# Performance work log

Hardware: AMD Instinct MI355X
Metric: run time of the kernel (lower is better)

## Reference

```python
import jax, jax.numpy as jnp
import numpy as np

M = 8          # ensemble size
B = 16384      # batch
HIST = 5       # history
L = 384        # latent_dim
A = 1          # action_dim
HID = 512      # hidden_dim
NHL = 2        # num_hidden_layers
DIN = L * HIST + A * HIST  # 1925
EPS = 1e-5     # BatchNorm eps


def setup_inputs() -> dict:
    key = jax.random.key(0)
    ks = jax.random.split(key, 6)
    w = lambda k, shape: (jax.random.normal(k, shape, jnp.float32) * 0.02)
    return {
        "z_hist": jax.random.normal(ks[0], (B, HIST, L), jnp.float32),
        "a_hist": jax.random.normal(ks[1], (B, HIST, A), jnp.float32),
        # per-model parameters, stacked along leading ensemble dim M
        "W1": w(ks[2], (M, DIN, HID)),
        "b1": jnp.zeros((M, HID), jnp.float32),
        "Wh": w(ks[3], (NHL, M, HID, HID)),
        "bh": jnp.zeros((NHL, M, HID), jnp.float32),
        "gamma": jnp.ones((NHL, M, HID), jnp.float32),
        "beta": jnp.zeros((NHL, M, HID), jnp.float32),
        "rmean": jnp.zeros((NHL, M, HID), jnp.float32),   # BN running mean (eval mode)
        "rvar": jnp.ones((NHL, M, HID), jnp.float32),      # BN running var (eval mode)
        "W3": w(ks[4], (M, HID, L)),
        "b3": jnp.zeros((M, L), jnp.float32),
    }


def reference(z_hist, a_hist, W1, b1, Wh, bh, gamma, beta, rmean, rvar, W3, b3):
    # EnsembleTransitionModel.forward, batched over the ensemble dim instead of
    # a Python loop over models. BatchNorm in eval mode; Dropout inactive (eval).
    bsz = z_hist.shape[0]
    x = jnp.concatenate([z_hist.reshape(bsz, -1), a_hist.reshape(bsz, -1)], axis=1)  # [B, DIN]
    # input projection + ReLU: [M, B, HID]
    h = jax.nn.relu(jnp.einsum('bi,mih->mbh', x, W1) + b1[:, None, :])
    n_layers = Wh.shape[0]
    for l in range(n_layers):  # small fixed structural loop (num_hidden_layers)
        h = jnp.einsum('mbh,mhk->mbk', h, Wh[l]) + bh[l][:, None, :]
        h = (h - rmean[l][:, None, :]) * jax.lax.rsqrt(rvar[l][:, None, :] + EPS)
        h = jax.nn.relu(h * gamma[l][:, None, :] + beta[l][:, None, :])
    delta = jnp.einsum('mbh,mhl->mbl', h, W3) + b3[:, None, :]
    # residual: pred_z = z_t + delta, broadcast over ensemble dim
    return delta + z_hist[:, -1, :][None, :, :]
```

## Files before the change

kernel.cpp:

```cpp
#include <hip/hip_runtime.h>
#include <hip/hip_bf16.h>

#define M_ENS 8
#define BATCH 16384
#define HIST 5
#define LDIM 384
#define HID 512
#define NHL 2
#define DIN 1925
#define KP 2048

typedef unsigned short u16;
typedef unsigned int u32;
typedef __attribute__((ext_vector_type(8))) short bf16x8;
typedef __attribute__((ext_vector_type(4))) float f32x4;

__device__ __forceinline__ u16 f2b(float f) {
    u32 u = __builtin_bit_cast(u32, f);
    u32 r = (u + 0x7fffu + ((u >> 16) & 1u)) >> 16;
    return (u16)r;
}

#define BARRIER asm volatile("s_barrier" ::: "memory")

__global__ void build_x(const float* __restrict__ z, const float* __restrict__ a,
                        u16* __restrict__ xp) {
    int idx = blockIdx.x * 256 + threadIdx.x;
    int b = idx / (KP / 2);
    int k2 = (idx % (KP / 2)) * 2;
    if (b >= BATCH) return;
    u32 packed = 0;
#pragma unroll
    for (int j = 0; j < 2; ++j) {
        int k = k2 + j;
        float v = 0.f;
        if (k < HIST * LDIM) v = z[(size_t)b * (HIST * LDIM) + k];
        else if (k < DIN)    v = a[b * HIST + (k - HIST * LDIM)];
        packed |= ((u32)f2b(v)) << (16 * j);
    }
    *(u32*)(&xp[(size_t)b * KP + k2]) = packed;
}

__global__ void transpose_cvt(const float* __restrict__ in, u16* __restrict__ out,
                              int R, int C, int Rp) {
    __shared__ float tile[32][33];
    const float* inb = in + (size_t)blockIdx.z * R * C;
    u16* outb = out + (size_t)blockIdx.z * C * Rp;
    int r0 = blockIdx.x * 32, c0 = blockIdx.y * 32;
    int tx = threadIdx.x & 31, ty = threadIdx.x >> 5;
#pragma unroll
    for (int i = 0; i < 32; i += 8) {
        int r = r0 + ty + i;
        float v = 0.f;
        if (r < R) v = inb[(size_t)r * C + c0 + tx];
        tile[ty + i][tx] = v;
    }
    __syncthreads();
#pragma unroll
    for (int i = 0; i < 32; i += 8) {
        outb[(size_t)(c0 + ty + i) * Rp + r0 + tx] = f2b(tile[tx][ty + i]);
    }
}

__global__ void make_tables(const float* __restrict__ bh, const float* __restrict__ gamma,
                            const float* __restrict__ beta, const float* __restrict__ rmean,
                            const float* __restrict__ rvar, float* __restrict__ s,
                            float* __restrict__ t, int n) {
    int i = blockIdx.x * 256 + threadIdx.x;
    if (i >= n) return;
    float inv = rsqrtf(rvar[i] + 1e-5f);
    float sc = gamma[i] * inv;
    s[i] = sc;
    t[i] = (bh[i] - rmean[i]) * sc + beta[i];
}

template <int MODE>
__global__ __launch_bounds__(512, 2) void gemm8p(
    const u16* __restrict__ A, const u16* __restrict__ Bw,
    const float* __restrict__ Sv, const float* __restrict__ Tv,
    u16* __restrict__ Ho, int K) {
    extern __shared__ char smem[];
    const int tid = threadIdx.x;
    const int lane = tid & 63;
    const int wid = tid >> 6;
    const int wm = wid >> 2;
    const int wn = wid & 3;

    int rowT, colT, mI;
    const u16 *Ab, *Bb;
    int lda, ldb;
    if (MODE == 0) {
        int xcd = blockIdx.x & 7, i = blockIdx.x >> 3;
        rowT = i >> 1; colT = xcd * 2 + (i & 1);
        Ab = A; lda = KP;
        Bb = Bw + (size_t)colT * 256 * KP; ldb = KP;
        mI = 0;
    } else {
        const int nwg = gridDim.x;
        const int swz = (blockIdx.x & 7) * (nwg >> 3) + (blockIdx.x >> 3);
        mI = swz >> 7;
        int rem = swz & 127;
        rowT = rem >> 1; colT = rem & 1;
        Ab = A + (size_t)mI * BATCH * HID; lda = HID;
        Bb = Bw + (size_t)mI * HID * HID + (size_t)colT * 256 * HID; ldb = HID;
    }
    const int rowBase = rowT * 256;
    const int NT = K >> 6;

    auto STAGE = [&](int par, int op, int half, int tk) {
#pragma unroll
        for (int i = 0; i < 2; ++i) {
            int ii = wid * 2 + i;
            int row = ii * 8 + (lane >> 3);
            int gc = lane & 7;
            const u16* src;
            if (op == 0)
                src = Ab + (size_t)(rowBase + half * 128 + row) * lda + tk * 64 + ((gc ^ (row & 7)) << 3);
            else
                src = Bb + (size_t)(half * 128 + row) * ldb + tk * 64 + ((gc ^ (row & 7)) << 3);
            u16* dst = (u16*)(smem + par * 65536 + op * 32768 + half * 16384) + (size_t)(ii * 64 + lane) * 8;
            __builtin_amdgcn_global_load_lds((const __attribute__((address_space(1))) void*)src,
                                             (__attribute__((address_space(3))) void*)dst, 16, 0, 0);
        }
    };

    const int laneRow = lane & 15;
    int xg[2];
    xg[0] = (((lane >> 4)) ^ (lane & 7)) << 4;
    xg[1] = ((4 | (lane >> 4)) ^ (lane & 7)) << 4;
#define RDF(base, r, kk) (*(const bf16x8*)((base) + (size_t)(r) * 128 + xg[kk]))

    f32x4 acc[8][4] = {};
    bf16x8 af[4][2], bfr[4][2];
    const int bcol0 = (wn & 1) * 64;

    STAGE(0, 1, 0, 0); STAGE(0, 1, 1, 0);
    STAGE(0, 0, 0, 0); STAGE(0, 0, 1, 0);
    if (NT > 1) { STAGE(1, 1, 0, 1); STAGE(1, 1, 1, 1); }
    asm volatile("s_waitcnt vmcnt(4)" ::: "memory");
    BARRIER;

    for (int T = 0; T < NT; ++T) {
        const int p = T & 1;
        const char* pA = smem + p * 65536 + wm * 16384;
        const char* pB = smem + p * 65536 + 32768 + (wn >> 1) * 16384;

#pragma unroll
        for (int mf = 0; mf < 4; ++mf) {
            af[mf][0] = RDF(pA, mf * 16 + laneRow, 0);
            af[mf][1] = RDF(pA, mf * 16 + laneRow, 1);
        }
#pragma unroll
        for (int nf = 0; nf < 2; ++nf) {
            bfr[nf][0] = RDF(pB, bcol0 + nf * 16 + laneRow, 0);
            bfr[nf][1] = RDF(pB, bcol0 + nf * 16 + laneRow, 1);
        }
        if (T + 1 < NT) STAGE((T + 1) & 1, 0, 0, T + 1);
        BARRIER;
        __builtin_amdgcn_s_setprio(1);
#pragma unroll
        for (int kk = 0; kk < 2; ++kk)
#pragma unroll
            for (int mf = 0; mf < 4; ++mf)
#pragma unroll
                for (int nf = 0; nf < 2; ++nf)
                    acc[mf][nf] = __builtin_amdgcn_mfma_f32_16x16x32_bf16(af[mf][kk], bfr[nf][kk], acc[mf][nf], 0, 0, 0);
        __builtin_amdgcn_s_setprio(0);
        BARRIER;

#pragma unroll
        for (int nf = 2; nf < 4; ++nf) {
            bfr[nf][0] = RDF(pB, bcol0 + nf * 16 + laneRow, 0);
            bfr[nf][1] = RDF(pB, bcol0 + nf * 16 + laneRow, 1);
        }
        if (T + 1 < NT) STAGE((T + 1) & 1, 0, 1, T + 1);
        BARRIER;
        __builtin_amdgcn_s_setprio(1);
#pragma unroll
        for (int kk = 0; kk < 2; ++kk)
#pragma unroll
            for (int mf = 0; mf < 4; ++mf)
#pragma unroll
                for (int nf = 2; nf < 4; ++nf)
                    acc[mf][nf] = __builtin_amdgcn_mfma_f32_16x16x32_bf16(af[mf][kk], bfr[nf][kk], acc[mf][nf], 0, 0, 0);
        __builtin_amdgcn_s_setprio(0);
        BARRIER;

#pragma unroll
        for (int mf = 0; mf < 4; ++mf) {
            af[mf][0] = RDF(pA, (4 + mf) * 16 + laneRow, 0);
            af[mf][1] = RDF(pA, (4 + mf) * 16 + laneRow, 1);
        }
        if (T + 2 < NT) STAGE(p, 1, 0, T + 2);
        BARRIER;
        __builtin_amdgcn_s_setprio(1);
#pragma unroll
        for (int kk = 0; kk < 2; ++kk)
#pragma unroll
            for (int mf = 0; mf < 4; ++mf)
#pragma unroll
                for (int nf = 2; nf < 4; ++nf)
                    acc[4 + mf][nf] = __builtin_amdgcn_mfma_f32_16x16x32_bf16(af[mf][kk], bfr[nf][kk], acc[4 + mf][nf], 0, 0, 0);
        __builtin_amdgcn_s_setprio(0);
        BARRIER;

        if (T + 2 < NT) {
            STAGE(p, 1, 1, T + 2);
            asm volatile("s_waitcnt vmcnt(4)" ::: "memory");
        } else {
            asm volatile("s_waitcnt vmcnt(0)" ::: "memory");
        }
        BARRIER;
        __builtin_amdgcn_s_setprio(1);
#pragma unroll
        for (int kk = 0; kk < 2; ++kk)
#pragma unroll
            for (int mf = 0; mf < 4; ++mf)
#pragma unroll
                for (int nf = 0; nf < 2; ++nf)
                    acc[4 + mf][nf] = __builtin_amdgcn_mfma_f32_16x16x32_bf16(af[mf][kk], bfr[nf][kk], acc[4 + mf][nf], 0, 0, 0);
        __builtin_amdgcn_s_setprio(0);
        BARRIER;
    }

#pragma unroll
    for (int mf = 0; mf < 8; ++mf) {
        int row = rowBase + wm * 128 + mf * 16 + ((lane >> 4) << 2);
#pragma unroll
        for (int nf = 0; nf < 4; ++nf) {
            int c = colT * 256 + wn * 64 + nf * 16 + (lane & 15);
            if (MODE == 0) {
                float tb = Tv[c];
                size_t base = (size_t)(c >> 9) * BATCH * HID + (c & 511);
#pragma unroll
                for (int q = 0; q < 4; ++q) {
                    float v = acc[mf][nf][q] + tb;
                    Ho[base + (size_t)(row + q) * HID] = f2b(v > 0.f ? v : 0.f);
                }
            } else {
                float sc = Sv[mI * HID + c], tb = Tv[mI * HID + c];
                u16* H = Ho + (size_t)mI * BATCH * HID;
#pragma unroll
                for (int q = 0; q < 4; ++q) {
                    float v = acc[mf][nf][q] * sc + tb;
                    H[(size_t)(row + q) * HID + c] = f2b(v > 0.f ? v : 0.f);
                }
            }
        }
    }
}

__global__ __launch_bounds__(512, 1) void h2out(
    const u16* __restrict__ h1, const u16* __restrict__ Wh2,
    const float* __restrict__ Sv, const float* __restrict__ Tv,
    const u16* __restrict__ W3p, const float* __restrict__ b3,
    const float* __restrict__ zres, float* __restrict__ out) {
    extern __shared__ char smem[];
    const int tid = threadIdx.x;
    const int lane = tid & 63;
    const int wid = tid >> 6;
    const int wm = wid >> 2;
    const int wn = wid & 3;
    const int m = blockIdx.x & 7;
    const int rowBase = (blockIdx.x >> 3) * 128;
    const int lr15 = lane & 15;

    const u16* Ab = h1 + ((size_t)m * BATCH + rowBase) * HID;
    const u16* Bb = Wh2 + (size_t)m * HID * HID;
    const u16* W3b = W3p + (size_t)m * LDIM * HID;
    const float* b3b = b3 + m * LDIM;

    int xg[2];
    xg[0] = (((lane >> 4)) ^ (lane & 7)) << 4;
    xg[1] = ((4 | (lane >> 4)) ^ (lane & 7)) << 4;

    auto stA = [&](int par, int tk) {
#pragma unroll
        for (int i = 0; i < 2; ++i) {
            int ii = wid * 2 + i;
            int row = ii * 8 + (lane >> 3);
            int gc = lane & 7;
            const u16* src = Ab + (size_t)row * HID + tk * 64 + ((gc ^ (row & 7)) << 3);
            u16* dst = (u16*)(smem + par * 16384) + (size_t)(ii * 64 + lane) * 8;
            __builtin_amdgcn_global_load_lds((const __attribute__((address_space(1))) void*)src,
                                             (__attribute__((address_space(3))) void*)dst, 16, 0, 0);
        }
    };
    auto stB = [&](int par, int q, int tk) {
#pragma unroll
        for (int i = 0; i < 2; ++i) {
            int ii = wid * 2 + i;
            int row = ii * 8 + (lane >> 3);
            int gc = lane & 7;
            const u16* src = Bb + (size_t)(q * 128 + row) * HID + tk * 64 + ((gc ^ (row & 7)) << 3);
            u16* dst = (u16*)(smem + 32768 + par * 65536 + q * 16384) + (size_t)(ii * 64 + lane) * 8;
            __builtin_amdgcn_global_load_lds((const __attribute__((address_space(1))) void*)src,
                                             (__attribute__((address_space(3))) void*)dst, 16, 0, 0);
        }
    };

    f32x4 acc[4][8] = {};
    bf16x8 afr[4][2];
    const int NT = HID / 64;

    stA(0, 0); stB(0, 0, 0); stB(0, 1, 0); stB(0, 2, 0); stB(0, 3, 0);
    asm volatile("s_waitcnt vmcnt(0)" ::: "memory");
    BARRIER;

    for (int T = 0; T < NT; ++T) {
        const int p = T & 1;
        const char* pA = smem + p * 16384;
        const char* qb = smem + 32768 + p * 65536 + wn * 16384;

#pragma unroll
        for (int mf = 0; mf < 4; ++mf) {
            int lr = wm * 64 + mf * 16 + lr15;
            afr[mf][0] = RDF(pA, lr, 0);
            afr[mf][1] = RDF(pA, lr, 1);
        }
        bf16x8 b01[2][2];
#pragma unroll
        for (int nf = 0; nf < 2; ++nf) {
            b01[nf][0] = RDF(qb, nf * 16 + lr15, 0);
            b01[nf][1] = RDF(qb, nf * 16 + lr15, 1);
        }
        if (T + 1 < NT) stA(p ^ 1, T + 1);
        BARRIER;
        __builtin_amdgcn_s_setprio(1);
#pragma unroll
        for (int kk = 0; kk < 2; ++kk)
#pragma unroll
            for (int mf = 0; mf < 4; ++mf)
#pragma unroll
                for (int nf = 0; nf < 2; ++nf)
                    acc[mf][nf] = __builtin_amdgcn_mfma_f32_16x16x32_bf16(afr[mf][kk], b01[nf][kk], acc[mf][nf], 0, 0, 0);
        __builtin_amdgcn_s_setprio(0);
        BARRIER;

#pragma unroll
        for (int nf = 0; nf < 2; ++nf) {
            b01[nf][0] = RDF(qb, (2 + nf) * 16 + lr15, 0);
            b01[nf][1] = RDF(qb, (2 + nf) * 16 + lr15, 1);
        }
        if (T + 1 < NT) { stB(p ^ 1, 0, T + 1); stB(p ^ 1, 1, T + 1); }
        BARRIER;
        __builtin_amdgcn_s_setprio(1);
#pragma unroll
        for (int kk = 0; kk < 2; ++kk)
#pragma unroll
            for (int mf = 0; mf < 4; ++mf)
#pragma unroll
                for (int nf = 0; nf < 2; ++nf)
                    acc[mf][2 + nf] = __builtin_amdgcn_mfma_f32_16x16x32_bf16(afr[mf][kk], b01[nf][kk], acc[mf][2 + nf], 0, 0, 0);
        __builtin_amdgcn_s_setprio(0);
        BARRIER;

#pragma unroll
        for (int nf = 0; nf < 2; ++nf) {
            b01[nf][0] = RDF(qb, (4 + nf) * 16 + lr15, 0);
            b01[nf][1] = RDF(qb, (4 + nf) * 16 + lr15, 1);
        }
        if (T + 1 < NT) { stB(p ^ 1, 2, T + 1); stB(p ^ 1, 3, T + 1); }
        BARRIER;
        __builtin_amdgcn_s_setprio(1);
#pragma unroll
        for (int kk = 0; kk < 2; ++kk)
#pragma unroll
            for (int mf = 0; mf < 4; ++mf)
#pragma unroll
                for (int nf = 0; nf < 2; ++nf)
                    acc[mf][4 + nf] = __builtin_amdgcn_mfma_f32_16x16x32_bf16(afr[mf][kk], b01[nf][kk], acc[mf][4 + nf], 0, 0, 0);
        __builtin_amdgcn_s_setprio(0);
        BARRIER;

#pragma unroll
        for (int nf = 0; nf < 2; ++nf) {
            b01[nf][0] = RDF(qb, (6 + nf) * 16 + lr15, 0);
            b01[nf][1] = RDF(qb, (6 + nf) * 16 + lr15, 1);
        }
        if (T + 2 < NT) {
            stA(p, T + 2);
            asm volatile("s_waitcnt vmcnt(2)" ::: "memory");
        } else {
            asm volatile("s_waitcnt vmcnt(0)" ::: "memory");
        }
        BARRIER;
        __builtin_amdgcn_s_setprio(1);
#pragma unroll
        for (int kk = 0; kk < 2; ++kk)
#pragma unroll
            for (int mf = 0; mf < 4; ++mf)
#pragma unroll
                for (int nf = 0; nf < 2; ++nf)
                    acc[mf][6 + nf] = __builtin_amdgcn_mfma_f32_16x16x32_bf16(afr[mf][kk], b01[nf][kk], acc[mf][6 + nf], 0, 0, 0);
        __builtin_amdgcn_s_setprio(0);
        BARRIER;
    }

#pragma unroll
    for (int mf = 0; mf < 4; ++mf) {
#pragma unroll
        for (int nf = 0; nf < 8; ++nf) {
            int col = wn * 128 + nf * 16 + lr15;
            float sc = Sv[m * HID + col], tt = Tv[m * HID + col];
#pragma unroll
            for (int q = 0; q < 4; ++q) {
                int row = wm * 64 + mf * 16 + ((lane >> 4) << 2) + q;
                float v = acc[mf][nf][q] * sc + tt;
                v = v > 0.f ? v : 0.f;
                *(u16*)(smem + 32768 + row * 1024 + (((col >> 3) ^ (row & 7)) << 4) + ((col & 7) << 1)) = f2b(v);
            }
        }
    }
    asm volatile("s_waitcnt lgkmcnt(0)" ::: "memory");
    BARRIER;

    bf16x8 w3r[3];
#pragma unroll
    for (int j = 0; j < 3; ++j) {
        int gi = tid * 3 + j;
        w3r[j] = *(const bf16x8*)(W3b + (size_t)(gi >> 2) * HID + ((gi & 3) << 3));
    }
    f32x4 acc2[4][6] = {};
    for (int t = 0; t < 16; ++t) {
#pragma unroll
        for (int j = 0; j < 3; ++j) {
            int gi = tid * 3 + j;
            *(bf16x8*)(smem + (gi >> 2) * 64 + (((gi & 3) ^ ((gi >> 2) & 3)) << 4)) = w3r[j];
        }
        if (t + 1 < 16) {
#pragma unroll
            for (int j = 0; j < 3; ++j) {
                int gi = tid * 3 + j;
                w3r[j] = *(const bf16x8*)(W3b + (size_t)(gi >> 2) * HID + (t + 1) * 32 + ((gi & 3) << 3));
            }
        }
        asm volatile("s_waitcnt lgkmcnt(0)" ::: "memory");
        BARRIER;
        bf16x8 a1[4], b1r[6];
#pragma unroll
        for (int mf = 0; mf < 4; ++mf) {
            int r = wm * 64 + mf * 16 + lr15;
            a1[mf] = *(const bf16x8*)(smem + 32768 + r * 1024 + (((4 * t + (lane >> 4)) ^ (lane & 7)) << 4));
        }
#pragma unroll
        for (int nf = 0; nf < 6; ++nf) {
            int r3 = wn * 96 + nf * 16 + lr15;
            b1r[nf] = *(const bf16x8*)(smem + r3 * 64 + (((lane >> 4) ^ (r3 & 3)) << 4));
        }
        __builtin_amdgcn_s_setprio(1);
#pragma unroll
        for (int mf = 0; mf < 4; ++mf)
#pragma unroll
            for (int nf = 0; nf < 6; ++nf)
                acc2[mf][nf] = __builtin_amdgcn_mfma_f32_16x16x32_bf16(a1[mf], b1r[nf], acc2[mf][nf], 0, 0, 0);
        __builtin_amdgcn_s_setprio(0);
        BARRIER;
    }

#pragma unroll
    for (int mf = 0; mf < 4; ++mf) {
#pragma unroll
        for (int nf = 0; nf < 6; ++nf) {
            int c = wn * 96 + nf * 16 + lr15;
            float bv = b3b[c];
#pragma unroll
            for (int q = 0; q < 4; ++q) {
                int grow = rowBase + wm * 64 + mf * 16 + ((lane >> 4) << 2) + q;
                out[((size_t)m * BATCH + grow) * LDIM + c] =
                    acc2[mf][nf][q] + bv + zres[(size_t)grow * (HIST * LDIM) + (HIST - 1) * LDIM + c];
            }
        }
    }
}

template <int MODE>
__global__ __launch_bounds__(256, 2) void gemm_bt(
    const u16* __restrict__ A, size_t aStride, int lda,
    const u16* __restrict__ Bt, size_t bStride,
    const float* __restrict__ Sv, const float* __restrict__ Tv, int ptStride,
    u16* __restrict__ Ho, size_t hStride,
    float* __restrict__ Fo, size_t fStride,
    const float* __restrict__ Zres,
    int K, int m0) {
    __shared__ u16 As[128 * 64];
    __shared__ u16 Bs[128 * 64];

    const int tid = threadIdx.x;
    const int lane = tid & 63;
    const int wid = tid >> 6;
    const int wr = (wid >> 1) * 64;
    const int wc = (wid & 1) * 64;
    const int z = blockIdx.z;
    const int rowBase = blockIdx.x * 128;
    const int colBase = blockIdx.y * 128;

    const u16* Ab = A + (size_t)z * aStride;
    const u16* Bb = Bt + (size_t)z * bStride;

    f32x4 acc[4][4] = {};

    int aoff[4], boff[4];
#pragma unroll
    for (int f = 0; f < 4; ++f) {
        int ar = wr + f * 16 + (lane & 15);
        aoff[f] = (ar * 128 + ((lane >> 4) * 16)) ^ ((ar & 7) << 4);
        int br = wc + f * 16 + (lane & 15);
        boff[f] = (br * 128 + ((lane >> 4) * 16)) ^ ((br & 7) << 4);
    }

    for (int k0 = 0; k0 < K; k0 += 64) {
#pragma unroll
        for (int i = 0; i < 4; ++i) {
            int gg = i * 256 + tid;
            int row = gg >> 3, gc = gg & 7;
            const u16* srcA = Ab + (size_t)(rowBase + row) * lda + k0 + ((gc ^ (row & 7)) << 3);
            __builtin_amdgcn_global_load_lds(
                (const __attribute__((address_space(1))) void*)srcA,
                (__attribute__((address_space(3))) void*)(As + gg * 8), 16, 0, 0);
            const u16* srcB = Bb + (size_t)(colBase + row) * K + k0 + ((gc ^ (row & 7)) << 3);
            __builtin_amdgcn_global_load_lds(
                (const __attribute__((address_space(1))) void*)srcB,
                (__attribute__((address_space(3))) void*)(Bs + gg * 8), 16, 0, 0);
        }
        __syncthreads();
#pragma unroll
        for (int kk = 0; kk < 2; ++kk) {
            bf16x8 af[4], bfr[4];
#pragma unroll
            for (int f = 0; f < 4; ++f) {
                af[f]  = *(const bf16x8*)((const char*)As + (aoff[f] ^ (kk << 6)));
                bfr[f] = *(const bf16x8*)((const char*)Bs + (boff[f] ^ (kk << 6)));
            }
#pragma unroll
            for (int i = 0; i < 4; ++i)
#pragma unroll
                for (int j = 0; j < 4; ++j)
                    acc[i][j] = __builtin_amdgcn_mfma_f32_16x16x32_bf16(af[i], bfr[j], acc[i][j], 0, 0, 0);
        }
        __syncthreads();
    }

    const int mg = m0 + z;
#pragma unroll
    for (int i = 0; i < 4; ++i) {
        int rbase = rowBase + wr + i * 16 + ((lane >> 4) << 2);
#pragma unroll
        for (int j = 0; j < 4; ++j) {
            int n = colBase + wc + j * 16 + (lane & 15);
            if (MODE == 0) {
                float bias = Tv[(size_t)mg * ptStride + n];
                u16* H = Ho + (size_t)z * hStride;
#pragma unroll
                for (int q = 0; q < 4; ++q) {
                    float v = acc[i][j][q] + bias;
                    v = v > 0.f ? v : 0.f;
                    H[(size_t)(rbase + q) * HID + n] = f2b(v);
                }
            } else if (MODE == 1) {
                float sc = Sv[(size_t)mg * ptStride + n];
                float tt = Tv[(size_t)mg * ptStride + n];
                u16* H = Ho + (size_t)z * hStride;
#pragma unroll
                for (int q = 0; q < 4; ++q) {
                    float v = acc[i][j][q] * sc + tt;
                    v = v > 0.f ? v : 0.f;
                    H[(size_t)(rbase + q) * HID + n] = f2b(v);
                }
            } else {
                float bias = Tv[(size_t)mg * ptStride + n];
                float* F = Fo + (size_t)z * fStride;
#pragma unroll
                for (int q = 0; q < 4; ++q) {
                    int b = rbase + q;
                    float v = acc[i][j][q] + bias + Zres[(size_t)b * (HIST * LDIM) + (HIST - 1) * LDIM + n];
                    F[(size_t)b * LDIM + n] = v;
                }
            }
        }
    }
}

extern "C" void kernel_launch(void* const* d_in, const int* in_sizes, int n_in,
                              void* d_out, int out_size, void* d_ws, size_t ws_size,
                              hipStream_t stream) {
    const float* z_hist = (const float*)d_in[0];
    const float* a_hist = (const float*)d_in[1];
    const float* W1    = (const float*)d_in[2];
    const float* b1    = (const float*)d_in[3];
    const float* Wh    = (const float*)d_in[4];
    const float* bh    = (const float*)d_in[5];
    const float* gamma = (const float*)d_in[6];
    const float* beta  = (const float*)d_in[7];
    const float* rmean = (const float*)d_in[8];
    const float* rvar  = (const float*)d_in[9];
    const float* W3    = (const float*)d_in[10];
    const float* b3    = (const float*)d_in[11];
    float* out = (float*)d_out;

    char* ws = (char*)d_ws;
    size_t off = 0;
    auto alloc = [&](size_t bytes) {
        void* p = ws + off;
        off = (off + bytes + 255) & ~(size_t)255;
        return p;
    };
    u16* xp  = (u16*)alloc((size_t)BATCH * KP * 2);
    u16* W1t = (u16*)alloc((size_t)M_ENS * HID * KP * 2);
    u16* Wht = (u16*)alloc((size_t)NHL * M_ENS * HID * HID * 2);
    u16* W3t = (u16*)alloc((size_t)M_ENS * LDIM * HID * 2);
    float* stab = (float*)alloc((size_t)NHL * M_ENS * HID * 4);
    float* ttab = (float*)alloc((size_t)NHL * M_ENS * HID * 4);
    size_t fixed = off;
    size_t hFull = (size_t)M_ENS * BATCH * HID * 2;
    bool full = (fixed + 2 * hFull <= ws_size);
    int MC = full ? M_ENS : 1;
    u16* h0 = (u16*)alloc((size_t)MC * BATCH * HID * 2);
    u16* h1 = (u16*)alloc((size_t)MC * BATCH * HID * 2);

    {
        int total = BATCH * KP / 2;
        build_x<<<(total + 255) / 256, 256, 0, stream>>>(z_hist, a_hist, xp);
        dim3 g1(KP / 32, HID / 32, M_ENS);
        transpose_cvt<<<g1, 256, 0, stream>>>(W1, W1t, DIN, HID, KP);
        dim3 g2(HID / 32, HID / 32, NHL * M_ENS);
        transpose_cvt<<<g2, 256, 0, stream>>>(Wh, Wht, HID, HID, HID);
        dim3 g3(HID / 32, LDIM / 32, M_ENS);
        transpose_cvt<<<g3, 256, 0, stream>>>(W3, W3t, HID, LDIM, HID);
        int n = NHL * M_ENS * HID;
        make_tables<<<(n + 255) / 256, 256, 0, stream>>>(bh, gamma, beta, rmean, rvar, stab, ttab, n);
    }

    if (full) {
        (void)hipFuncSetAttribute(reinterpret_cast<const void*>(&gemm8p<0>),
                                  hipFuncAttributeMaxDynamicSharedMemorySize, 131072);
        (void)hipFuncSetAttribute(reinterpret_cast<const void*>(&gemm8p<1>),
                                  hipFuncAttributeMaxDynamicSharedMemorySize, 131072);
        (void)hipFuncSetAttribute(reinterpret_cast<const void*>(&h2out),
                                  hipFuncAttributeMaxDynamicSharedMemorySize, 163840);
        gemm8p<0><<<1024, 512, 131072, stream>>>(xp, W1t, nullptr, b1, h0, KP);
        gemm8p<1><<<1024, 512, 131072, stream>>>(h0, Wht, stab, ttab, h1, HID);
        h2out<<<1024, 512, 163840, stream>>>(
            h1, Wht + (size_t)M_ENS * HID * HID,
            stab + M_ENS * HID, ttab + M_ENS * HID,
            W3t, b3, z_hist, out);
    } else {
        for (int m0 = 0; m0 < M_ENS; m0 += MC) {
            dim3 grid(BATCH / 128, HID / 128, MC);
            gemm_bt<0><<<grid, 256, 0, stream>>>(
                xp, 0, KP,
                W1t + (size_t)m0 * HID * KP, (size_t)HID * KP,
                nullptr, b1, HID,
                h0, (size_t)BATCH * HID, nullptr, 0, nullptr,
                KP, m0);
            for (int l = 0; l < NHL; ++l) {
                u16* hin = l ? h1 : h0;
                u16* hout = l ? h0 : h1;
                gemm_bt<1><<<grid, 256, 0, stream>>>(
                    hin, (size_t)BATCH * HID, HID,
                    Wht + ((size_t)l * M_ENS + m0) * HID * HID, (size_t)HID * HID,
                    stab + (size_t)l * M_ENS * HID, ttab + (size_t)l * M_ENS * HID, HID,
                    hout, (size_t)BATCH * HID, nullptr, 0, nullptr,
                    HID, m0);
            }
            dim3 gridO(BATCH / 128, LDIM / 128, MC);
            gemm_bt<2><<<gridO, 256, 0, stream>>>(
                h0, (size_t)BATCH * HID, HID,
                W3t + (size_t)m0 * LDIM * HID, (size_t)LDIM * HID,
                nullptr, b3, LDIM,
                nullptr, 0,
                out + (size_t)m0 * BATCH * LDIM, (size_t)BATCH * LDIM,
                z_hist,
                HID, m0);
        }
    }
}
```

Before: 626.5 us.

## Replace layer-1 pipelined 256x256 GEMM with simple 128x128 tile kernel

The first-layer GEMM (x[B,2048] times W1 for all 8 models, N=4096) moves from the double-buffered 256x256-tile gemm8p<0> with 512 threads to a new l1_bt kernel. The new kernel uses 128x128 tiles, 256 threads, static shared memory, 2 blocks per CU and an XCD-aware tile mapping. This trades the software pipelining and larger reuse per tile for smaller tiles, more blocks and better occupancy. The change also drops MODE 0 from gemm8p, adds a GLL macro, and changes one m0 argument in the fallback path from m0 to 0.

```diff
diff --git a/kernel.cpp b/kernel.cpp
--- a/kernel.cpp
+++ b/kernel.cpp
@@ -22,6 +22,9 @@
 }
 
 #define BARRIER asm volatile("s_barrier" ::: "memory")
+#define GLL(src, dst) __builtin_amdgcn_global_load_lds( \
+    (const __attribute__((address_space(1))) void*)(src), \
+    (__attribute__((address_space(3))) void*)(dst), 16, 0, 0)
 
 __global__ void build_x(const float* __restrict__ z, const float* __restrict__ a,
                         u16* __restrict__ xp) {
@@ -72,6 +75,84 @@
     float sc = gamma[i] * inv;
     s[i] = sc;
     t[i] = (bh[i] - rmean[i]) * sc + beta[i];
+}
+
+__global__ __launch_bounds__(256, 2) void l1_bt(
+    const u16* __restrict__ xp, const u16* __restrict__ W1t,
+    const float* __restrict__ b1, u16* __restrict__ Ho) {
+    __shared__ u16 As[128 * 64];
+    __shared__ u16 Bs[128 * 64];
+
+    const int tid = threadIdx.x;
+    const int lane = tid & 63;
+    const int wid = tid >> 6;
+    const int wr = (wid >> 1) * 64;
+    const int wc = (wid & 1) * 64;
+
+    const int bid = blockIdx.x;
+    const int xcd = bid & 7, i = bid >> 3;
+    const int colT = xcd * 4 + (i & 3);
+    const int rowT = i >> 2;
+    const int rowBase = rowT * 128;
+    const int colBase = colT * 128;
+
+    const u16* Ab = xp + (size_t)rowBase * KP;
+    const u16* Bb = W1t + (size_t)colBase * KP;
+
+    f32x4 acc[4][4] = {};
+
+    int aoff[4], boff[4];
+#pragma unroll
+    for (int f = 0; f < 4; ++f) {
+        int ar = wr + f * 16 + (lane & 15);
+        aoff[f] = (ar * 128 + ((lane >> 4) * 16)) ^ ((ar & 7) << 4);
+        int br = wc + f * 16 + (lane & 15);
+        boff[f] = (br * 128 + ((lane >> 4) * 16)) ^ ((br & 7) << 4);
+    }
+
+    for (int k0 = 0; k0 < KP; k0 += 64) {
+#pragma unroll
+        for (int s = 0; s < 4; ++s) {
+            int gg = s * 256 + tid;
+            int row = gg >> 3, gc = gg & 7;
+            const u16* srcA = Ab + (size_t)row * KP + k0 + ((gc ^ (row & 7)) << 3);
+            GLL(srcA, As + gg * 8);
+            const u16* srcB = Bb + (size_t)row * KP + k0 + ((gc ^ (row & 7)) << 3);
+            GLL(srcB, Bs + gg * 8);
+        }
+        __syncthreads();
+#pragma unroll
+        for (int kk = 0; kk < 2; ++kk) {
+            bf16x8 af[4], bfr[4];
+#pragma unroll
+            for (int f = 0; f < 4; ++f) {
+                af[f]  = *(const bf16x8*)((const char*)As + (aoff[f] ^ (kk << 6)));
+                bfr[f] = *(const bf16x8*)((const char*)Bs + (boff[f] ^ (kk << 6)));
+            }
+#pragma unroll
+            for (int a = 0; a < 4; ++a)
+#pragma unroll
+                for (int b = 0; b < 4; ++b)
+                    acc[a][b] = __builtin_amdgcn_mfma_f32_16x16x32_bf16(af[a], bfr[b], acc[a][b], 0, 0, 0);
+        }
+        __syncthreads();
+    }
+
+#pragma unroll
+    for (int a = 0; a < 4; ++a) {
+        int rbase = rowBase + wr + a * 16 + ((lane >> 4) << 2);
+#pragma unroll
+        for (int b = 0; b < 4; ++b) {
+            int c = colBase + wc + b * 16 + (lane & 15);
+            float tb = b1[c];
+            size_t base = (size_t)(c >> 9) * BATCH * HID + (c & 511);
+#pragma unroll
+            for (int q = 0; q < 4; ++q) {
+                float v = acc[a][b][q] + tb;
+                Ho[base + (size_t)(rbase + q) * HID] = f2b(v > 0.f ? v : 0.f);
+            }
+        }
+    }
 }
 
 template <int MODE>
@@ -86,24 +167,14 @@
     const int wm = wid >> 2;
     const int wn = wid & 3;
 
-    int rowT, colT, mI;
-    const u16 *Ab, *Bb;
-    int lda, ldb;
-    if (MODE == 0) {
-        int xcd = blockIdx.x & 7, i = blockIdx.x >> 3;
-        rowT = i >> 1; colT = xcd * 2 + (i & 1);
-        Ab = A; lda = KP;
-        Bb = Bw + (size_t)colT * 256 * KP; ldb = KP;
-        mI = 0;
-    } else {
-        const int nwg = gridDim.x;
-        const int swz = (blockIdx.x & 7) * (nwg >> 3) + (blockIdx.x >> 3);
-        mI = swz >> 7;
-        int rem = swz & 127;
-        rowT = rem >> 1; colT = rem & 1;
-        Ab = A + (size_t)mI * BATCH * HID; lda = HID;
-        Bb = Bw + (size_t)mI * HID * HID + (size_t)colT * 256 * HID; ldb = HID;
-    }
+    const int nwg = gridDim.x;
+    const int swz = (blockIdx.x & 7) * (nwg >> 3) + (blockIdx.x >> 3);
+    const int mI = swz >> 7;
+    const int rem = swz & 127;
+    const int rowT = rem >> 1, colT = rem & 1;
+    const u16* Ab = A + (size_t)mI * BATCH * HID;
+    const u16* Bb = Bw + (size_t)mI * HID * HID + (size_t)colT * 256 * HID;
+    const int lda = HID, ldb = HID;
     const int rowBase = rowT * 256;
     const int NT = K >> 6;
 
@@ -119,8 +190,7 @@
             else
                 src = Bb + (size_t)(half * 128 + row) * ldb + tk * 64 + ((gc ^ (row & 7)) << 3);
             u16* dst = (u16*)(smem + par * 65536 + op * 32768 + half * 16384) + (size_t)(ii * 64 + lane) * 8;
-            __builtin_amdgcn_global_load_lds((const __attribute__((address_space(1))) void*)src,
-                                             (__attribute__((address_space(3))) void*)dst, 16, 0, 0);
+            GLL(src, dst);
         }
     };
 
@@ -229,22 +299,12 @@
 #pragma unroll
         for (int nf = 0; nf < 4; ++nf) {
             int c = colT * 256 + wn * 64 + nf * 16 + (lane & 15);
-            if (MODE == 0) {
-                float tb = Tv[c];
-                size_t base = (size_t)(c >> 9) * BATCH * HID + (c & 511);
-#pragma unroll
-                for (int q = 0; q < 4; ++q) {
-                    float v = acc[mf][nf][q] + tb;
-                    Ho[base + (size_t)(row + q) * HID] = f2b(v > 0.f ? v : 0.f);
-                }
-            } else {
-                float sc = Sv[mI * HID + c], tb = Tv[mI * HID + c];
-                u16* H = Ho + (size_t)mI * BATCH * HID;
-#pragma unroll
-                for (int q = 0; q < 4; ++q) {
-                    float v = acc[mf][nf][q] * sc + tb;
-                    H[(size_t)(row + q) * HID + c] = f2b(v > 0.f ? v : 0.f);
-                }
+            float sc = Sv[mI * HID + c], tb = Tv[mI * HID + c];
+            u16* H = Ho + (size_t)mI * BATCH * HID;
+#pragma unroll
+            for (int q = 0; q < 4; ++q) {
+                float v = acc[mf][nf][q] * sc + tb;
+                H[(size_t)(row + q) * HID + c] = f2b(v > 0.f ? v : 0.f);
             }
         }
     }
@@ -282,8 +342,7 @@
             int gc = lane & 7;
             const u16* src = Ab + (size_t)row * HID + tk * 64 + ((gc ^ (row & 7)) << 3);
             u16* dst = (u16*)(smem + par * 16384) + (size_t)(ii * 64 + lane) * 8;
-            __builtin_amdgcn_global_load_lds((const __attribute__((address_space(1))) void*)src,
-                                             (__attribute__((address_space(3))) void*)dst, 16, 0, 0);
+            GLL(src, dst);
         }
     };
     auto stB = [&](int par, int q, int tk) {
@@ -294,8 +353,7 @@
             int gc = lane & 7;
             const u16* src = Bb + (size_t)(q * 128 + row) * HID + tk * 64 + ((gc ^ (row & 7)) << 3);
             u16* dst = (u16*)(smem + 32768 + par * 65536 + q * 16384) + (size_t)(ii * 64 + lane) * 8;
-            __builtin_amdgcn_global_load_lds((const __attribute__((address_space(1))) void*)src,
-                                             (__attribute__((address_space(3))) void*)dst, 16, 0, 0);
+            GLL(src, dst);
         }
     };
 
@@ -515,13 +573,9 @@
             int gg = i * 256 + tid;
             int row = gg >> 3, gc = gg & 7;
             const u16* srcA = Ab + (size_t)(rowBase + row) * lda + k0 + ((gc ^ (row & 7)) << 3);
-            __builtin_amdgcn_global_load_lds(
-                (const __attribute__((address_space(1))) void*)srcA,
-                (__attribute__((address_space(3))) void*)(As + gg * 8), 16, 0, 0);
+            GLL(srcA, As + gg * 8);
             const u16* srcB = Bb + (size_t)(colBase + row) * K + k0 + ((gc ^ (row & 7)) << 3);
-            __builtin_amdgcn_global_load_lds(
-                (const __attribute__((address_space(1))) void*)srcB,
-                (__attribute__((address_space(3))) void*)(Bs + gg * 8), 16, 0, 0);
+            GLL(srcB, Bs + gg * 8);
         }
         __syncthreads();
 #pragma unroll
@@ -632,13 +686,11 @@
     }
 
     if (full) {
-        (void)hipFuncSetAttribute(reinterpret_cast<const void*>(&gemm8p<0>),
-                                  hipFuncAttributeMaxDynamicSharedMemorySize, 131072);
         (void)hipFuncSetAttribute(reinterpret_cast<const void*>(&gemm8p<1>),
                                   hipFuncAttributeMaxDynamicSharedMemorySize, 131072);
         (void)hipFuncSetAttribute(reinterpret_cast<const void*>(&h2out),
                                   hipFuncAttributeMaxDynamicSharedMemorySize, 163840);
-        gemm8p<0><<<1024, 512, 131072, stream>>>(xp, W1t, nullptr, b1, h0, KP);
+        l1_bt<<<4096, 256, 0, stream>>>(xp, W1t, b1, h0);
         gemm8p<1><<<1024, 512, 131072, stream>>>(h0, Wht, stab, ttab, h1, HID);
         h2out<<<1024, 512, 163840, stream>>>(
             h1, Wht + (size_t)M_ENS * HID * HID,
@@ -671,7 +723,7 @@
                 nullptr, 0,
                 out + (size_t)m0 * BATCH * LDIM, (size_t)BATCH * LDIM,
                 z_hist,
-                HID, m0);
-        }
-    }
-}
+                HID, 0);
+        }
+    }
+}
```

Result: slower. 659.6 us (+5.3%).
